# Optimization experiments

Hardware: AMD Instinct MI355X
Metric: run time of the kernel (lower is better)

## Reference

```python
import jax, jax.numpy as jnp
import numpy as np

DIM = 96
HEADS = 6
WS = 8                      # window_size
OWS = int(WS * 0.5) + WS    # overlap_win_size = 12
PAD = (OWS - WS) // 2       # 2
Dd = Hh = Ww = 24
B = 1
L = Dd * Hh * Ww
MLP_H = DIM * 2
TBL = (WS + OWS - 1) ** 3   # 6859 relative-position-bias entries


def setup_inputs() -> dict:
    key = jax.random.key(0)
    ks = jax.random.split(key, 8)
    def n(k, shape, s=0.02):
        return jax.random.normal(k, shape, jnp.float32) * s
    return {
        "x": jax.random.normal(ks[0], (B, L, DIM), jnp.float32),
        "ln1_w": jnp.ones((DIM,), jnp.float32),
        "ln1_b": jnp.zeros((DIM,), jnp.float32),
        "qkv_w": n(ks[1], (3 * DIM, DIM)),
        "qkv_b": jnp.zeros((3 * DIM,), jnp.float32),
        "rpb": n(ks[2], (TBL, HEADS)),
        "proj_w": n(ks[3], (DIM, DIM)),
        "proj_b": jnp.zeros((DIM,), jnp.float32),
        "ln2_w": jnp.ones((DIM,), jnp.float32),
        "ln2_b": jnp.zeros((DIM,), jnp.float32),
        "fc1_w": n(ks[4], (MLP_H, DIM)),
        "fc1_b": jnp.zeros((MLP_H,), jnp.float32),
        "fc2_w": n(ks[5], (DIM, MLP_H)),
        "fc2_b": jnp.zeros((DIM,), jnp.float32),
        "rpi": jax.random.randint(ks[6], (WS ** 3, OWS ** 3), 0, TBL),
        "D": Dd, "H": Hh, "W": Ww,
    }


def _ln(x, w, b):
    m = jnp.mean(x, -1, keepdims=True)
    v = jnp.var(x, -1, keepdims=True)
    return (x - m) / jnp.sqrt(v + 1e-5) * w + b


def _ocab3d(x, ln1_w, ln1_b, qkv_w, qkv_b, rpb, proj_w, proj_b,
            ln2_w, ln2_b, fc1_w, fc1_b, fc2_w, fc2_b, rpi, D, H, W):
    Bz, Lz, C = x.shape
    hd = C // HEADS
    scale = hd ** -0.5
    shortcut = x

    xn = _ln(x, ln1_w, ln1_b).reshape(Bz, D, H, W, C)
    qkv = xn @ qkv_w.T + qkv_b                   # [B,D,H,W,3C]
    q = qkv[..., :C]
    kv = qkv[..., C:]                            # cat(k, v) on channels, [B,D,H,W,2C]

    nD, nH, nW = D // WS, H // WS, W // WS
    nw = nD * nH * nW

    # non-overlapping query windows -> [B*nw, WS^3, C]
    qw = q.reshape(Bz, nD, WS, nH, WS, nW, WS, C)
    qw = qw.transpose(0, 1, 3, 5, 2, 4, 6, 7).reshape(Bz * nw, WS ** 3, C)

    # overlapping kv windows via pad + strided gather (mirrors F.pad + unfold)
    kvp = jnp.pad(kv, ((0, 0), (PAD, PAD), (PAD, PAD), (PAD, PAD), (0, 0)))
    idx_d = (jnp.arange(nD) * WS)[:, None] + jnp.arange(OWS)[None, :]
    idx_h = (jnp.arange(nH) * WS)[:, None] + jnp.arange(OWS)[None, :]
    idx_w = (jnp.arange(nW) * WS)[:, None] + jnp.arange(OWS)[None, :]
    kw = kvp[:, idx_d]                 # [B,nD,OWS,Hp,Wp,2C]
    kw = kw[:, :, :, idx_h]            # [B,nD,OWS,nH,OWS,Wp,2C]
    kw = kw[:, :, :, :, :, idx_w]      # [B,nD,OWS,nH,OWS,nW,OWS,2C]
    kw = kw.transpose(0, 1, 3, 5, 2, 4, 6, 7).reshape(Bz * nw, OWS ** 3, 2 * C)
    kk, vv = kw[..., :C], kw[..., C:]

    qh = qw.reshape(-1, WS ** 3, HEADS, hd).transpose(0, 2, 1, 3) * scale
    kh = kk.reshape(-1, OWS ** 3, HEADS, hd).transpose(0, 2, 1, 3)
    vh = vv.reshape(-1, OWS ** 3, HEADS, hd).transpose(0, 2, 1, 3)

    attn = jnp.einsum('bhqd,bhkd->bhqk', qh, kh)               # [B*nw,H,512,1728]
    bias = rpb[rpi.reshape(-1)].reshape(WS ** 3, OWS ** 3, HEADS).transpose(2, 0, 1)
    attn = jax.nn.softmax(attn + bias[None], axis=-1)
    out = jnp.einsum('bhqk,bhkd->bhqd', attn, vh)
    out = out.transpose(0, 2, 1, 3).reshape(Bz * nw, WS ** 3, C)

    # window reverse -> [B, L, C]
    out = out.reshape(Bz, nD, nH, nW, WS, WS, WS, C)
    out = out.transpose(0, 1, 4, 2, 5, 3, 6, 7).reshape(Bz, D * H * W, C)

    x2 = out @ proj_w.T + proj_b + shortcut
    h1 = jax.nn.gelu(_ln(x2, ln2_w, ln2_b) @ fc1_w.T + fc1_b, approximate=False)
    return x2 + (h1 @ fc2_w.T + fc2_b)


def reference(x, ln1_w, ln1_b, qkv_w, qkv_b, rpb, proj_w, proj_b,
              ln2_w, ln2_b, fc1_w, fc1_b, fc2_w, fc2_b, rpi, D, H, W):
    return _ocab3d(x, ln1_w, ln1_b, qkv_w, qkv_b, rpb, proj_w, proj_b,
                   ln2_w, ln2_b, fc1_w, fc1_b, fc2_w, fc2_b, rpi, D, H, W)
```

## Files before the change

### kernel.cpp

```cpp
#include <hip/hip_runtime.h>
#include <math.h>

#define DIMC   96
#define NHEADS 6
#define HD     16
#define WSZ    8
#define OWSZ   12
#define PADW   2
#define DD     24
#define LTOK   13824
#define NWIN   27
#define NKEY   1728
#define NROW   512
#define MLPH   192
#define PDIM   28
#define PD3    21952
#define KVPN   (NHEADS*PD3*32)
#define TBL    6859

typedef __attribute__((ext_vector_type(4))) short bf16x4;
typedef __attribute__((ext_vector_type(8))) short bf16x8;
typedef __attribute__((ext_vector_type(4))) float f32x4;

__device__ __forceinline__ unsigned short bfround(float f) {
    unsigned u = __float_as_uint(f);
    return (unsigned short)((u + 0x7FFFu + ((u >> 16) & 1u)) >> 16);
}
__device__ __forceinline__ unsigned bfpack(float a, float b) {
    unsigned ua = __float_as_uint(a), ub = __float_as_uint(b);
    ua = (ua + 0x7FFFu + ((ua >> 16) & 1u)) >> 16;
    ub = (ub + 0x7FFFu + ((ub >> 16) & 1u)) >> 16;
    return ua | (ub << 16);
}
__device__ __forceinline__ uint4 pack8(const float* v) {
    uint4 u;
    u.x = bfpack(v[0], v[1]); u.y = bfpack(v[2], v[3]);
    u.z = bfpack(v[4], v[5]); u.w = bfpack(v[6], v[7]);
    return u;
}
__device__ __forceinline__ bf16x4 pack4(f32x4 p) {
    union { uint2 u; bf16x4 v; } r;
    r.u.x = __builtin_amdgcn_perm(__float_as_uint(p[1]), __float_as_uint(p[0]), 0x07060302u);
    r.u.y = __builtin_amdgcn_perm(__float_as_uint(p[3]), __float_as_uint(p[2]), 0x07060302u);
    return r.v;
}
__device__ __forceinline__ f32x4 mfma16(bf16x4 a, bf16x4 b, f32x4 c) {
#if __has_builtin(__builtin_amdgcn_mfma_f32_16x16x16bf16_1k)
    return __builtin_amdgcn_mfma_f32_16x16x16bf16_1k(a, b, c, 0, 0, 0);
#else
    bf16x8 a8 = {a[0], a[1], a[2], a[3], 0, 0, 0, 0};
    bf16x8 b8 = {b[0], b[1], b[2], b[3], 0, 0, 0, 0};
    return __builtin_amdgcn_mfma_f32_16x16x32_bf16(a8, b8, c, 0, 0, 0);
#endif
}

__global__ void zero_kernel(float4* __restrict__ p, int n4) {
    int i = blockIdx.x * blockDim.x + threadIdx.x;
    if (i < n4) p[i] = make_float4(0.f, 0.f, 0.f, 0.f);
}

__global__ __launch_bounds__(256) void rpbT_kernel(
        const float* __restrict__ rpb, float* __restrict__ rpbT) {
    int i = blockIdx.x * 256 + threadIdx.x;
    if (i < TBL) {
        #pragma unroll
        for (int h = 0; h < NHEADS; ++h) rpbT[h * TBL + i] = rpb[i * NHEADS + h];
    }
}

template<int KT, int NCHUNKS, int MODE, bool LN>
__global__ __launch_bounds__(256) void gemm_kernel(
        const float* __restrict__ X, const float* __restrict__ W,
        const float* __restrict__ bias, const float* __restrict__ lnw,
        const float* __restrict__ lnb, const float* __restrict__ res,
        void* __restrict__ out, void* __restrict__ out2) {
    constexpr int K = KT * 32;
    __shared__ uint4 Af4[2 * KT * 4 * 16];
    __shared__ uint4 Bf4[6 * KT * 4 * 16];
    int tid  = threadIdx.x;
    int row0 = blockIdx.x * 32;

    if (tid < 128) {
        int row = tid >> 2, part = tid & 3;
        int rt = row >> 4, mm = row & 15;
        const float* xr = X + (long)(row0 + row) * K + part * (K / 4);
        if (LN) {
            float v[24];
            const float4* xp = (const float4*)xr;
            float s = 0.f, sq = 0.f;
            #pragma unroll
            for (int i = 0; i < 6; ++i) {
                float4 t = xp[i];
                v[i*4+0] = t.x; v[i*4+1] = t.y; v[i*4+2] = t.z; v[i*4+3] = t.w;
                s  += t.x + t.y + t.z + t.w;
                sq += t.x*t.x + t.y*t.y + t.z*t.z + t.w*t.w;
            }
            s  += __shfl_xor(s, 1);  s  += __shfl_xor(s, 2);
            sq += __shfl_xor(sq, 1); sq += __shfl_xor(sq, 2);
            float mean = s * (1.f / 96.f);
            float inv  = rsqrtf(sq * (1.f / 96.f) - mean * mean + 1e-5f);
            const float4* wp = (const float4*)(lnw + part * 24);
            const float4* bp = (const float4*)(lnb + part * 24);
            #pragma unroll
            for (int i = 0; i < 6; ++i) {
                float4 wv = wp[i], bv = bp[i];
                v[i*4+0] = (v[i*4+0] - mean) * inv * wv.x + bv.x;
                v[i*4+1] = (v[i*4+1] - mean) * inv * wv.y + bv.y;
                v[i*4+2] = (v[i*4+2] - mean) * inv * wv.z + bv.z;
                v[i*4+3] = (v[i*4+3] - mean) * inv * wv.w + bv.w;
            }
            #pragma unroll
            for (int gg = 0; gg < 3; ++gg) {
                int g = part * 3 + gg;
                int kt = g >> 2, qq = g & 3;
                Af4[((rt * KT + kt) * 4 + qq) * 16 + mm] = pack8(v + gg * 8);
            }
        } else {
            #pragma unroll
            for (int gg = 0; gg < KT; ++gg) {
                const float4* xp = (const float4*)(xr + gg * 8);
                float v[8];
                float4 t0 = xp[0], t1 = xp[1];
                v[0]=t0.x; v[1]=t0.y; v[2]=t0.z; v[3]=t0.w;
                v[4]=t1.x; v[5]=t1.y; v[6]=t1.z; v[7]=t1.w;
                int g = part * KT + gg;
                int kt = g >> 2, qq = g & 3;
                Af4[((rt * KT + kt) * 4 + qq) * 16 + mm] = pack8(v);
            }
        }
    }

    int wave = tid >> 6, lane = tid & 63;
    int qq = lane >> 4, mI = lane & 15;
    int rt = wave & 1, cg = wave >> 1;

    for (int nc = 0; nc < NCHUNKS; ++nc) {
        if (nc) __syncthreads();
        for (int idx = tid; idx < 96 * 4 * KT; idx += 256) {
            int n = idx / (4 * KT);
            int g = idx % (4 * KT);
            const float4* wp = (const float4*)(W + (long)(nc * 96 + n) * K + g * 8);
            float v[8];
            float4 t0 = wp[0], t1 = wp[1];
            v[0]=t0.x; v[1]=t0.y; v[2]=t0.z; v[3]=t0.w;
            v[4]=t1.x; v[5]=t1.y; v[6]=t1.z; v[7]=t1.w;
            int ct = n >> 4, nn = n & 15, kt = g >> 2, qg = g & 3;
            Bf4[((ct * KT + kt) * 4 + qg) * 16 + nn] = pack8(v);
        }
        __syncthreads();

        f32x4 acc[3];
        #pragma unroll
        for (int j = 0; j < 3; ++j) acc[j] = (f32x4){0.f, 0.f, 0.f, 0.f};
        #pragma unroll
        for (int kt = 0; kt < KT; ++kt) {
            bf16x8 a = *(const bf16x8*)&Af4[((rt * KT + kt) * 4 + qq) * 16 + mI];
            #pragma unroll
            for (int j = 0; j < 3; ++j) {
                bf16x8 b = *(const bf16x8*)&Bf4[(((cg * 3 + j) * KT + kt) * 4 + qq) * 16 + mI];
                acc[j] = __builtin_amdgcn_mfma_f32_16x16x32_bf16(a, b, acc[j], 0, 0, 0);
            }
        }

        float bv[3];
        #pragma unroll
        for (int j = 0; j < 3; ++j) bv[j] = bias[nc * 96 + (cg * 3 + j) * 16 + mI];
        #pragma unroll
        for (int r = 0; r < 4; ++r) {
            int row = row0 + rt * 16 + qq * 4 + r;
            if (MODE == 0) {
                if (nc == 0) {
                    unsigned short* op = (unsigned short*)out + (long)row * 96;
                    #pragma unroll
                    for (int j = 0; j < 3; ++j)
                        op[(cg * 3 + j) * 16 + mI] = bfround(0.25f * (acc[j][r] + bv[j]));
                } else {
                    int d = row / 576, hh = (row / 24) % 24, w2 = row % 24;
                    long pos = ((long)(d + 2) * 28 + (hh + 2)) * 28 + (w2 + 2);
                    #pragma unroll
                    for (int j = 0; j < 3; ++j) {
                        int head = cg * 3 + j;
                        ((unsigned short*)out2)[((long)head * PD3 + pos) * 32 +
                            (nc == 2 ? 16 : 0) + mI] = bfround(acc[j][r] + bv[j]);
                    }
                }
            } else if (MODE == 1 || MODE == 3) {
                const float* rp = res + (long)row * 96;
                float* op = (float*)out + (long)row * 96;
                #pragma unroll
                for (int j = 0; j < 3; ++j)
                    op[(cg * 3 + j) * 16 + mI] = acc[j][r] + bv[j] + rp[(cg * 3 + j) * 16 + mI];
            } else {
                float* op = (float*)out + (long)row * 192 + nc * 96;
                #pragma unroll
                for (int j = 0; j < 3; ++j) {
                    float v = acc[j][r] + bv[j];
                    op[(cg * 3 + j) * 16 + mI] = 0.5f * v * (1.f + erff(v * 0.70710678f));
                }
            }
        }
    }
}

__global__ __launch_bounds__(256) void bias_kernel(
        const int* __restrict__ rpi, const float* __restrict__ rpbT,
        unsigned short* __restrict__ biasP) {
    int b = blockIdx.x, head = b / 108, kt = b % 108;
    const float* tab = rpbT + head * TBL;
    int k0 = kt * 16;
    #pragma unroll
    for (int qq = 0; qq < 2; ++qq) {
        int qi = threadIdx.x * 2 + qq;
        const int* rp = rpi + (long)qi * NKEY + k0;
        int idx[16];
        #pragma unroll
        for (int j = 0; j < 4; ++j) {
            int4 t = *(const int4*)(rp + j * 4);
            idx[j*4+0] = t.x; idx[j*4+1] = t.y; idx[j*4+2] = t.z; idx[j*4+3] = t.w;
        }
        #pragma unroll
        for (int quad = 0; quad < 4; ++quad) {
            ushort4 v;
            v.x = bfround(tab[idx[quad*4+0]]);
            v.y = bfround(tab[idx[quad*4+1]]);
            v.z = bfround(tab[idx[quad*4+2]]);
            v.w = bfround(tab[idx[quad*4+3]]);
            *(ushort4*)(biasP + ((((long)head*108 + kt)*4 + quad)*512 + qi)*4) = v;
        }
    }
}

#define KSTR 20
#define VSTR 68
__global__ __launch_bounds__(256) void attn_kernel(
        const unsigned short* __restrict__ q, const unsigned short* __restrict__ kvp2,
        const unsigned short* __restrict__ biasP, float* __restrict__ ao) {
    __shared__ unsigned short Ks[2][64 * KSTR];
    __shared__ unsigned short Vs[2][16 * VSTR];
    int bid = blockIdx.x;
    int w = bid / 24, rem = bid % 24;
    int head = rem >> 2, quart = rem & 3;
    int wd8 = (w / 9) * 8, wh8 = ((w / 3) % 3) * 8, ww8 = (w % 3) * 8;
    int tid = threadIdx.x, wave = tid >> 6, lane = tid & 63;
    int quad = lane >> 4, m16 = lane & 15;
    int key = tid >> 2, part = tid & 3;

    auto kvaddr = [&](int c) -> const uint4* {
        int jg = c * 64 + key;
        int i = jg / 144, jh = (jg / 12) % 12, jw = jg % 12;
        long sp = ((long)(wd8 + i) * PDIM + (wh8 + jh)) * PDIM + (ww8 + jw);
        return (const uint4*)(kvp2 + ((long)head * PD3 + sp) * 32 + part * 8);
    };
    auto writeLDS = [&](int b, uint4 v) {
        if (part < 2) {
            *(uint2*)(&Ks[b][key * KSTR + part * 8])     = make_uint2(v.x, v.y);
            *(uint2*)(&Ks[b][key * KSTR + part * 8 + 4]) = make_uint2(v.z, v.w);
        } else {
            int d0 = (part - 2) * 8;
            Vs[b][(d0+0)*VSTR + key] = (unsigned short)(v.x);
            Vs[b][(d0+1)*VSTR + key] = (unsigned short)(v.x >> 16);
            Vs[b][(d0+2)*VSTR + key] = (unsigned short)(v.y);
            Vs[b][(d0+3)*VSTR + key] = (unsigned short)(v.y >> 16);
            Vs[b][(d0+4)*VSTR + key] = (unsigned short)(v.z);
            Vs[b][(d0+5)*VSTR + key] = (unsigned short)(v.z >> 16);
            Vs[b][(d0+6)*VSTR + key] = (unsigned short)(v.w);
            Vs[b][(d0+7)*VSTR + key] = (unsigned short)(v.w >> 16);
        }
    };

    int grow[2]; bf16x4 qf[2];
    #pragma unroll
    for (int qt = 0; qt < 2; ++qt) {
        int ql = quart * 128 + wave * 32 + qt * 16 + m16;
        int ld = ql >> 6, lh = (ql >> 3) & 7, lw = ql & 7;
        grow[qt] = ((wd8 + ld) * 24 + (wh8 + lh)) * 24 + (ww8 + lw);
        qf[qt] = *(const bf16x4*)(q + (long)grow[qt] * 96 + head * 16 + quad * 4);
    }

    const unsigned short* bbase = biasP + (long)head * 884736 + quad * 2048
                                 + ((quart * 128 + wave * 32 + m16) << 2);
    uint2 bcur[2][4];
    #pragma unroll
    for (int qt = 0; qt < 2; ++qt)
        #pragma unroll
        for (int kt = 0; kt < 4; ++kt)
            bcur[qt][kt] = *(const uint2*)(bbase + kt * 8192 + qt * 64);

    writeLDS(0, *kvaddr(0));

    f32x4 o[2];
    o[0] = (f32x4){0.f,0.f,0.f,0.f}; o[1] = (f32x4){0.f,0.f,0.f,0.f};
    float l[2] = {0.f, 0.f};
    uint4 stgn;

    #pragma unroll 1
    for (int c = 0; c < 27; ++c) {
        if (c + 1 < 27) stgn = *kvaddr(c + 1);
        __syncthreads();
        int b = c & 1;

        bf16x4 kf[4];
        #pragma unroll
        for (int kt = 0; kt < 4; ++kt)
            kf[kt] = *(const bf16x4*)(&Ks[b][(kt * 16 + m16) * KSTR + quad * 4]);

        f32x4 S[2][4];
        #pragma unroll
        for (int qt = 0; qt < 2; ++qt)
            #pragma unroll
            for (int kt = 0; kt < 4; ++kt) {
                uint2 bv = bcur[qt][kt];
                f32x4 ci;
                ci[0] = __uint_as_float(bv.x << 16);
                ci[1] = __uint_as_float(bv.x & 0xffff0000u);
                ci[2] = __uint_as_float(bv.y << 16);
                ci[3] = __uint_as_float(bv.y & 0xffff0000u);
                S[qt][kt] = mfma16(kf[kt], qf[qt], ci);
            }

        uint2 bnxt[2][4];
        if (c + 1 < 27) {
            const unsigned short* bp = bbase + (long)(c + 1) * 32768;
            #pragma unroll
            for (int qt = 0; qt < 2; ++qt)
                #pragma unroll
                for (int kt = 0; kt < 4; ++kt)
                    bnxt[qt][kt] = *(const uint2*)(bp + kt * 8192 + qt * 64);
        }

        #pragma unroll
        for (int qt = 0; qt < 2; ++qt) {
            float ls = 0.f;
            #pragma unroll
            for (int kt = 0; kt < 4; ++kt)
                #pragma unroll
                for (int r = 0; r < 4; ++r) {
                    float p = __expf(S[qt][kt][r]);
                    S[qt][kt][r] = p; ls += p;
                }
            l[qt] += ls;
        }

        #pragma unroll
        for (int kt = 0; kt < 4; ++kt) {
            bf16x4 vf = *(const bf16x4*)(&Vs[b][m16 * VSTR + kt * 16 + quad * 4]);
            o[0] = mfma16(vf, pack4(S[0][kt]), o[0]);
            o[1] = mfma16(vf, pack4(S[1][kt]), o[1]);
        }

        if (c + 1 < 27) writeLDS((c + 1) & 1, stgn);
        #pragma unroll
        for (int qt = 0; qt < 2; ++qt)
            #pragma unroll
            for (int kt = 0; kt < 4; ++kt) bcur[qt][kt] = bnxt[qt][kt];
    }

    #pragma unroll
    for (int qt = 0; qt < 2; ++qt) {
        float lq = l[qt];
        lq += __shfl_xor(lq, 16);
        lq += __shfl_xor(lq, 32);
        float inv = 1.f / lq;
        float4* op = (float4*)(ao + (long)grow[qt] * 96 + head * 16 + quad * 4);
        *op = make_float4(o[qt][0]*inv, o[qt][1]*inv, o[qt][2]*inv, o[qt][3]*inv);
    }
}

extern "C" void kernel_launch(void* const* d_in, const int* in_sizes, int n_in,
                              void* d_out, int out_size, void* d_ws, size_t ws_size,
                              hipStream_t stream) {
    const float* x     = (const float*)d_in[0];
    const float* ln1w  = (const float*)d_in[1];
    const float* ln1b  = (const float*)d_in[2];
    const float* qkvw  = (const float*)d_in[3];
    const float* qkvb  = (const float*)d_in[4];
    const float* rpb   = (const float*)d_in[5];
    const float* projw = (const float*)d_in[6];
    const float* projb = (const float*)d_in[7];
    const float* ln2w  = (const float*)d_in[8];
    const float* ln2b  = (const float*)d_in[9];
    const float* fc1w  = (const float*)d_in[10];
    const float* fc1b  = (const float*)d_in[11];
    const float* fc2w  = (const float*)d_in[12];
    const float* fc2b  = (const float*)d_in[13];
    const int*   rpi   = (const int*)d_in[14];
    float* outp = (float*)d_out;

    float* ws = (float*)d_ws;
    float*          ao    = ws;
    unsigned short* q16   = (unsigned short*)(ws + 1327104);
    unsigned short* kvp16 = (unsigned short*)(ws + 1990656);
    float*          hbuf  = ws + 4098048;
    unsigned short* biasP = (unsigned short*)hbuf;
    float*          rpbT  = ws + 6752256;
    float*          x2    = ao;

    {
        int n4 = KVPN * 2 / 16;
        zero_kernel<<<(n4 + 255) / 256, 256, 0, stream>>>((float4*)kvp16, n4);
    }
    rpbT_kernel<<<27, 256, 0, stream>>>(rpb, rpbT);
    gemm_kernel<3, 3, 0, true ><<<432, 256, 0, stream>>>(x,  qkvw, qkvb, ln1w, ln1b, nullptr, q16, kvp16);
    bias_kernel<<<NHEADS * 108, 256, 0, stream>>>(rpi, rpbT, biasP);
    attn_kernel<<<NWIN * NHEADS * 4, 256, 0, stream>>>(q16, kvp16, biasP, ao);
    gemm_kernel<3, 1, 1, false><<<432, 256, 0, stream>>>(ao, projw, projb, nullptr, nullptr, x, x2, nullptr);
    gemm_kernel<3, 2, 2, true ><<<432, 256, 0, stream>>>(x2, fc1w, fc1b, ln2w, ln2b, nullptr, hbuf, nullptr);
    gemm_kernel<6, 1, 3, false><<<432, 256, 0, stream>>>(hbuf, fc2w, fc2b, nullptr, nullptr, x2, outp, nullptr);
}
```

Measured before the change: 196.4 us.

## Split attention keys across two blocks and parallelize GEMM output chunks

The attention kernel now splits the 27 key chunks between two blocks per query tile. Each block writes an unnormalized output and row sums, and the projection GEMM combines the two halves and normalizes while loading its A tile. The gemm kernel moves its output-column chunks from a loop to separate blocks, the zero and rpb-transpose kernels merge into one launch, and the bias table is stored in fp32 instead of bf16. The aim is more blocks in flight and fewer launches, at the cost of doubled attention output traffic, a larger bias buffer, and repeated LN/A-tile loading per chunk.

Result: faster. 190.9 us (-2.8%).

```diff
diff --git a/kernel.cpp b/kernel.cpp
--- a/kernel.cpp
+++ b/kernel.cpp
@@ -17,6 +17,8 @@
 #define PD3    21952
 #define KVPN   (NHEADS*PD3*32)
 #define TBL    6859
+#define LSTR   82944
+#define AOSTR  1327104
 
 typedef __attribute__((ext_vector_type(4))) short bf16x4;
 typedef __attribute__((ext_vector_type(8))) short bf16x8;
@@ -54,39 +56,68 @@
 #endif
 }
 
-__global__ void zero_kernel(float4* __restrict__ p, int n4) {
-    int i = blockIdx.x * blockDim.x + threadIdx.x;
-    if (i < n4) p[i] = make_float4(0.f, 0.f, 0.f, 0.f);
-}
-
-__global__ __launch_bounds__(256) void rpbT_kernel(
-        const float* __restrict__ rpb, float* __restrict__ rpbT) {
-    int i = blockIdx.x * 256 + threadIdx.x;
-    if (i < TBL) {
-        #pragma unroll
-        for (int h = 0; h < NHEADS; ++h) rpbT[h * TBL + i] = rpb[i * NHEADS + h];
-    }
-}
-
-template<int KT, int NCHUNKS, int MODE, bool LN>
+#define ZBLK 2058
+__global__ __launch_bounds__(256) void init_kernel(
+        float4* __restrict__ kvz, const float* __restrict__ rpb,
+        float* __restrict__ rpbT) {
+    int bx = blockIdx.x;
+    if (bx < ZBLK) {
+        int i = bx * 256 + threadIdx.x;
+        if (i < KVPN * 2 / 16) kvz[i] = make_float4(0.f, 0.f, 0.f, 0.f);
+    } else {
+        int i = (bx - ZBLK) * 256 + threadIdx.x;
+        if (i < TBL) {
+            #pragma unroll
+            for (int h = 0; h < NHEADS; ++h) rpbT[h * TBL + i] = rpb[i * NHEADS + h];
+        }
+    }
+}
+
+template<int KT, int MODE, bool LN, int NSPLIT>
 __global__ __launch_bounds__(256) void gemm_kernel(
         const float* __restrict__ X, const float* __restrict__ W,
         const float* __restrict__ bias, const float* __restrict__ lnw,
         const float* __restrict__ lnb, const float* __restrict__ res,
+        const float* __restrict__ X2, const float* __restrict__ lbuf,
         void* __restrict__ out, void* __restrict__ out2) {
     constexpr int K = KT * 32;
     __shared__ uint4 Af4[2 * KT * 4 * 16];
     __shared__ uint4 Bf4[6 * KT * 4 * 16];
     int tid  = threadIdx.x;
-    int row0 = blockIdx.x * 32;
+    int nc   = blockIdx.x % NSPLIT;
+    int row0 = (blockIdx.x / NSPLIT) * 32;
 
     if (tid < 128) {
         int row = tid >> 2, part = tid & 3;
         int rt = row >> 4, mm = row & 15;
-        const float* xr = X + (long)(row0 + row) * K + part * (K / 4);
-        if (LN) {
+        if (MODE == 1) {
+            int grow = row0 + row;
+            const float4* a0 = (const float4*)(X  + (long)grow * 96 + part * 24);
+            const float4* a1 = (const float4*)(X2 + (long)grow * 96 + part * 24);
+            int ha = (part * 3) >> 1, hb = ha + 1;
+            float inva = 1.f / (lbuf[grow*6 + ha] + lbuf[LSTR + grow*6 + ha]);
+            float invb = 1.f / (lbuf[grow*6 + hb] + lbuf[LSTR + grow*6 + hb]);
             float v[24];
-            const float4* xp = (const float4*)xr;
+            #pragma unroll
+            for (int i = 0; i < 6; ++i) {
+                float4 u0 = a0[i], u1 = a1[i];
+                #pragma unroll
+                for (int j = 0; j < 4; ++j) {
+                    int gc = part * 24 + i * 4 + j;
+                    float lv = ((gc >> 4) == ha) ? inva : invb;
+                    float s = (j==0?u0.x+u1.x : j==1?u0.y+u1.y : j==2?u0.z+u1.z : u0.w+u1.w);
+                    v[i*4+j] = s * lv;
+                }
+            }
+            #pragma unroll
+            for (int gg = 0; gg < 3; ++gg) {
+                int g = part * 3 + gg;
+                int kt = g >> 2, qq = g & 3;
+                Af4[((rt * KT + kt) * 4 + qq) * 16 + mm] = pack8(v + gg * 8);
+            }
+        } else if (LN) {
+            float v[24];
+            const float4* xp = (const float4*)(X + (long)(row0 + row) * K + part * 24);
             float s = 0.f, sq = 0.f;
             #pragma unroll
             for (int i = 0; i < 6; ++i) {
@@ -116,6 +147,7 @@
                 Af4[((rt * KT + kt) * 4 + qq) * 16 + mm] = pack8(v + gg * 8);
             }
         } else {
+            const float* xr = X + (long)(row0 + row) * K + part * (K / 4);
             #pragma unroll
             for (int gg = 0; gg < KT; ++gg) {
                 const float4* xp = (const float4*)(xr + gg * 8);
@@ -130,73 +162,70 @@
         }
     }
 
+    for (int idx = tid; idx < 96 * 4 * KT; idx += 256) {
+        int n = idx / (4 * KT);
+        int g = idx % (4 * KT);
+        const float4* wp = (const float4*)(W + (long)(nc * 96 + n) * K + g * 8);
+        float v[8];
+        float4 t0 = wp[0], t1 = wp[1];
+        v[0]=t0.x; v[1]=t0.y; v[2]=t0.z; v[3]=t0.w;
+        v[4]=t1.x; v[5]=t1.y; v[6]=t1.z; v[7]=t1.w;
+        int ct = n >> 4, nn = n & 15, kt = g >> 2, qg = g & 3;
+        Bf4[((ct * KT + kt) * 4 + qg) * 16 + nn] = pack8(v);
+    }
+    __syncthreads();
+
     int wave = tid >> 6, lane = tid & 63;
     int qq = lane >> 4, mI = lane & 15;
     int rt = wave & 1, cg = wave >> 1;
 
-    for (int nc = 0; nc < NCHUNKS; ++nc) {
-        if (nc) __syncthreads();
-        for (int idx = tid; idx < 96 * 4 * KT; idx += 256) {
-            int n = idx / (4 * KT);
-            int g = idx % (4 * KT);
-            const float4* wp = (const float4*)(W + (long)(nc * 96 + n) * K + g * 8);
-            float v[8];
-            float4 t0 = wp[0], t1 = wp[1];
-            v[0]=t0.x; v[1]=t0.y; v[2]=t0.z; v[3]=t0.w;
-            v[4]=t1.x; v[5]=t1.y; v[6]=t1.z; v[7]=t1.w;
-            int ct = n >> 4, nn = n & 15, kt = g >> 2, qg = g & 3;
-            Bf4[((ct * KT + kt) * 4 + qg) * 16 + nn] = pack8(v);
-        }
-        __syncthreads();
-
-        f32x4 acc[3];
-        #pragma unroll
-        for (int j = 0; j < 3; ++j) acc[j] = (f32x4){0.f, 0.f, 0.f, 0.f};
-        #pragma unroll
-        for (int kt = 0; kt < KT; ++kt) {
-            bf16x8 a = *(const bf16x8*)&Af4[((rt * KT + kt) * 4 + qq) * 16 + mI];
-            #pragma unroll
-            for (int j = 0; j < 3; ++j) {
-                bf16x8 b = *(const bf16x8*)&Bf4[(((cg * 3 + j) * KT + kt) * 4 + qq) * 16 + mI];
-                acc[j] = __builtin_amdgcn_mfma_f32_16x16x32_bf16(a, b, acc[j], 0, 0, 0);
-            }
-        }
-
-        float bv[3];
-        #pragma unroll
-        for (int j = 0; j < 3; ++j) bv[j] = bias[nc * 96 + (cg * 3 + j) * 16 + mI];
-        #pragma unroll
-        for (int r = 0; r < 4; ++r) {
-            int row = row0 + rt * 16 + qq * 4 + r;
-            if (MODE == 0) {
-                if (nc == 0) {
-                    unsigned short* op = (unsigned short*)out + (long)row * 96;
-                    #pragma unroll
-                    for (int j = 0; j < 3; ++j)
-                        op[(cg * 3 + j) * 16 + mI] = bfround(0.25f * (acc[j][r] + bv[j]));
-                } else {
-                    int d = row / 576, hh = (row / 24) % 24, w2 = row % 24;
-                    long pos = ((long)(d + 2) * 28 + (hh + 2)) * 28 + (w2 + 2);
-                    #pragma unroll
-                    for (int j = 0; j < 3; ++j) {
-                        int head = cg * 3 + j;
-                        ((unsigned short*)out2)[((long)head * PD3 + pos) * 32 +
-                            (nc == 2 ? 16 : 0) + mI] = bfround(acc[j][r] + bv[j]);
-                    }
-                }
-            } else if (MODE == 1 || MODE == 3) {
-                const float* rp = res + (long)row * 96;
-                float* op = (float*)out + (long)row * 96;
+    f32x4 acc[3];
+    #pragma unroll
+    for (int j = 0; j < 3; ++j) acc[j] = (f32x4){0.f, 0.f, 0.f, 0.f};
+    #pragma unroll
+    for (int kt = 0; kt < KT; ++kt) {
+        bf16x8 a = *(const bf16x8*)&Af4[((rt * KT + kt) * 4 + qq) * 16 + mI];
+        #pragma unroll
+        for (int j = 0; j < 3; ++j) {
+            bf16x8 b = *(const bf16x8*)&Bf4[(((cg * 3 + j) * KT + kt) * 4 + qq) * 16 + mI];
+            acc[j] = __builtin_amdgcn_mfma_f32_16x16x32_bf16(a, b, acc[j], 0, 0, 0);
+        }
+    }
+
+    float bv[3];
+    #pragma unroll
+    for (int j = 0; j < 3; ++j) bv[j] = bias[nc * 96 + (cg * 3 + j) * 16 + mI];
+    #pragma unroll
+    for (int r = 0; r < 4; ++r) {
+        int row = row0 + rt * 16 + qq * 4 + r;
+        if (MODE == 0) {
+            if (nc == 0) {
+                unsigned short* op = (unsigned short*)out + (long)row * 96;
                 #pragma unroll
                 for (int j = 0; j < 3; ++j)
-                    op[(cg * 3 + j) * 16 + mI] = acc[j][r] + bv[j] + rp[(cg * 3 + j) * 16 + mI];
+                    op[(cg * 3 + j) * 16 + mI] = bfround(0.25f * (acc[j][r] + bv[j]));
             } else {
-                float* op = (float*)out + (long)row * 192 + nc * 96;
+                int d = row / 576, hh = (row / 24) % 24, w2 = row % 24;
+                long pos = ((long)(d + 2) * 28 + (hh + 2)) * 28 + (w2 + 2);
                 #pragma unroll
                 for (int j = 0; j < 3; ++j) {
-                    float v = acc[j][r] + bv[j];
-                    op[(cg * 3 + j) * 16 + mI] = 0.5f * v * (1.f + erff(v * 0.70710678f));
+                    int head = cg * 3 + j;
+                    ((unsigned short*)out2)[((long)head * PD3 + pos) * 32 +
+                        (nc == 2 ? 16 : 0) + mI] = bfround(acc[j][r] + bv[j]);
                 }
+            }
+        } else if (MODE == 1 || MODE == 3) {
+            const float* rp = res + (long)row * 96;
+            float* op = (float*)out + (long)row * 96;
+            #pragma unroll
+            for (int j = 0; j < 3; ++j)
+                op[(cg * 3 + j) * 16 + mI] = acc[j][r] + bv[j] + rp[(cg * 3 + j) * 16 + mI];
+        } else {
+            float* op = (float*)out + (long)row * 192 + nc * 96;
+            #pragma unroll
+            for (int j = 0; j < 3; ++j) {
+                float v = acc[j][r] + bv[j];
+                op[(cg * 3 + j) * 16 + mI] = 0.5f * v * (1.f + erff(v * 0.70710678f));
             }
         }
     }
@@ -204,29 +233,29 @@
 
 __global__ __launch_bounds__(256) void bias_kernel(
         const int* __restrict__ rpi, const float* __restrict__ rpbT,
-        unsigned short* __restrict__ biasP) {
-    int b = blockIdx.x, head = b / 108, kt = b % 108;
+        float* __restrict__ biasP) {
+    int bx = blockIdx.x;
+    int head = bx / 216;
+    int r2 = bx % 216;
+    int kt = r2 >> 1, qh = r2 & 1;
     const float* tab = rpbT + head * TBL;
     int k0 = kt * 16;
-    #pragma unroll
-    for (int qq = 0; qq < 2; ++qq) {
-        int qi = threadIdx.x * 2 + qq;
-        const int* rp = rpi + (long)qi * NKEY + k0;
-        int idx[16];
-        #pragma unroll
-        for (int j = 0; j < 4; ++j) {
-            int4 t = *(const int4*)(rp + j * 4);
-            idx[j*4+0] = t.x; idx[j*4+1] = t.y; idx[j*4+2] = t.z; idx[j*4+3] = t.w;
-        }
-        #pragma unroll
-        for (int quad = 0; quad < 4; ++quad) {
-            ushort4 v;
-            v.x = bfround(tab[idx[quad*4+0]]);
-            v.y = bfround(tab[idx[quad*4+1]]);
-            v.z = bfround(tab[idx[quad*4+2]]);
-            v.w = bfround(tab[idx[quad*4+3]]);
-            *(ushort4*)(biasP + ((((long)head*108 + kt)*4 + quad)*512 + qi)*4) = v;
-        }
+    int qi = qh * 256 + threadIdx.x;
+    const int* rp = rpi + (long)qi * NKEY + k0;
+    int idx[16];
+    #pragma unroll
+    for (int j = 0; j < 4; ++j) {
+        int4 t = *(const int4*)(rp + j * 4);
+        idx[j*4+0] = t.x; idx[j*4+1] = t.y; idx[j*4+2] = t.z; idx[j*4+3] = t.w;
+    }
+    #pragma unroll
+    for (int quad = 0; quad < 4; ++quad) {
+        float4 v;
+        v.x = tab[idx[quad*4+0]];
+        v.y = tab[idx[quad*4+1]];
+        v.z = tab[idx[quad*4+2]];
+        v.w = tab[idx[quad*4+3]];
+        *(float4*)(biasP + ((((long)head*108 + kt)*4 + quad)*512 + qi)*4) = v;
     }
 }
 
@@ -234,16 +263,20 @@
 #define VSTR 68
 __global__ __launch_bounds__(256) void attn_kernel(
         const unsigned short* __restrict__ q, const unsigned short* __restrict__ kvp2,
-        const unsigned short* __restrict__ biasP, float* __restrict__ ao) {
+        const float* __restrict__ biasP, float* __restrict__ ao,
+        float* __restrict__ lbuf) {
     __shared__ unsigned short Ks[2][64 * KSTR];
     __shared__ unsigned short Vs[2][16 * VSTR];
     int bid = blockIdx.x;
-    int w = bid / 24, rem = bid % 24;
-    int head = rem >> 2, quart = rem & 3;
+    int w = bid / 48, rem = bid % 48;
+    int head = rem >> 3;
+    int quart = (rem >> 1) & 3, half = rem & 1;
     int wd8 = (w / 9) * 8, wh8 = ((w / 3) % 3) * 8, ww8 = (w % 3) * 8;
     int tid = threadIdx.x, wave = tid >> 6, lane = tid & 63;
     int quad = lane >> 4, m16 = lane & 15;
     int key = tid >> 2, part = tid & 3;
+    int c0 = half ? 13 : 0;
+    int cn = half ? 14 : 13;
 
     auto kvaddr = [&](int c) -> const uint4* {
         int jg = c * 64 + key;
@@ -277,16 +310,16 @@
         qf[qt] = *(const bf16x4*)(q + (long)grow[qt] * 96 + head * 16 + quad * 4);
     }
 
-    const unsigned short* bbase = biasP + (long)head * 884736 + quad * 2048
-                                 + ((quart * 128 + wave * 32 + m16) << 2);
-    uint2 bcur[2][4];
+    const float* bbase = biasP + (long)head * 884736 + quad * 2048
+                         + ((quart * 128 + wave * 32 + m16) << 2);
+    f32x4 bcur[2][4];
     #pragma unroll
     for (int qt = 0; qt < 2; ++qt)
         #pragma unroll
         for (int kt = 0; kt < 4; ++kt)
-            bcur[qt][kt] = *(const uint2*)(bbase + kt * 8192 + qt * 64);
-
-    writeLDS(0, *kvaddr(0));
+            bcur[qt][kt] = *(const f32x4*)(bbase + (long)(c0*4 + kt) * 8192 + qt * 64);
+
+    writeLDS(0, *kvaddr(c0));
 
     f32x4 o[2];
     o[0] = (f32x4){0.f,0.f,0.f,0.f}; o[1] = (f32x4){0.f,0.f,0.f,0.f};
@@ -294,10 +327,11 @@
     uint4 stgn;
 
     #pragma unroll 1
-    for (int c = 0; c < 27; ++c) {
-        if (c + 1 < 27) stgn = *kvaddr(c + 1);
+    for (int cc = 0; cc < cn; ++cc) {
+        int c = c0 + cc;
+        if (cc + 1 < cn) stgn = *kvaddr(c + 1);
         __syncthreads();
-        int b = c & 1;
+        int b = cc & 1;
 
         bf16x4 kf[4];
         #pragma unroll
@@ -308,24 +342,17 @@
         #pragma unroll
         for (int qt = 0; qt < 2; ++qt)
             #pragma unroll
-            for (int kt = 0; kt < 4; ++kt) {
-                uint2 bv = bcur[qt][kt];
-                f32x4 ci;
-                ci[0] = __uint_as_float(bv.x << 16);
-                ci[1] = __uint_as_float(bv.x & 0xffff0000u);
-                ci[2] = __uint_as_float(bv.y << 16);
-                ci[3] = __uint_as_float(bv.y & 0xffff0000u);
-                S[qt][kt] = mfma16(kf[kt], qf[qt], ci);
-            }
-
-        uint2 bnxt[2][4];
-        if (c + 1 < 27) {
-            const unsigned short* bp = bbase + (long)(c + 1) * 32768;
+            for (int kt = 0; kt < 4; ++kt)
+                S[qt][kt] = mfma16(kf[kt], qf[qt], bcur[qt][kt]);
+
+        f32x4 bnxt[2][4];
+        if (cc + 1 < cn) {
+            const float* bp = bbase + (long)(c + 1) * 32768;
             #pragma unroll
             for (int qt = 0; qt < 2; ++qt)
                 #pragma unroll
                 for (int kt = 0; kt < 4; ++kt)
-                    bnxt[qt][kt] = *(const uint2*)(bp + kt * 8192 + qt * 64);
+                    bnxt[qt][kt] = *(const f32x4*)(bp + kt * 8192 + qt * 64);
         }
 
         #pragma unroll
@@ -348,21 +375,23 @@
             o[1] = mfma16(vf, pack4(S[1][kt]), o[1]);
         }
 
-        if (c + 1 < 27) writeLDS((c + 1) & 1, stgn);
+        if (cc + 1 < cn) writeLDS((cc + 1) & 1, stgn);
         #pragma unroll
         for (int qt = 0; qt < 2; ++qt)
             #pragma unroll
             for (int kt = 0; kt < 4; ++kt) bcur[qt][kt] = bnxt[qt][kt];
     }
 
+    float* aout = ao + (long)half * AOSTR;
+    float* lout = lbuf + (long)half * LSTR;
     #pragma unroll
     for (int qt = 0; qt < 2; ++qt) {
         float lq = l[qt];
         lq += __shfl_xor(lq, 16);
         lq += __shfl_xor(lq, 32);
-        float inv = 1.f / lq;
-        float4* op = (float4*)(ao + (long)grow[qt] * 96 + head * 16 + quad * 4);
-        *op = make_float4(o[qt][0]*inv, o[qt][1]*inv, o[qt][2]*inv, o[qt][3]*inv);
+        float4* op = (float4*)(aout + (long)grow[qt] * 96 + head * 16 + quad * 4);
+        *op = make_float4(o[qt][0], o[qt][1], o[qt][2], o[qt][3]);
+        if (quad == 0) lout[grow[qt] * 6 + head] = lq;
     }
 }
 
@@ -387,23 +416,20 @@
     float* outp = (float*)d_out;
 
     float* ws = (float*)d_ws;
-    float*          ao    = ws;
-    unsigned short* q16   = (unsigned short*)(ws + 1327104);
-    unsigned short* kvp16 = (unsigned short*)(ws + 1990656);
-    float*          hbuf  = ws + 4098048;
-    unsigned short* biasP = (unsigned short*)hbuf;
-    float*          rpbT  = ws + 6752256;
-    float*          x2    = ao;
-
-    {
-        int n4 = KVPN * 2 / 16;
-        zero_kernel<<<(n4 + 255) / 256, 256, 0, stream>>>((float4*)kvp16, n4);
-    }
-    rpbT_kernel<<<27, 256, 0, stream>>>(rpb, rpbT);
-    gemm_kernel<3, 3, 0, true ><<<432, 256, 0, stream>>>(x,  qkvw, qkvb, ln1w, ln1b, nullptr, q16, kvp16);
-    bias_kernel<<<NHEADS * 108, 256, 0, stream>>>(rpi, rpbT, biasP);
-    attn_kernel<<<NWIN * NHEADS * 4, 256, 0, stream>>>(q16, kvp16, biasP, ao);
-    gemm_kernel<3, 1, 1, false><<<432, 256, 0, stream>>>(ao, projw, projb, nullptr, nullptr, x, x2, nullptr);
-    gemm_kernel<3, 2, 2, true ><<<432, 256, 0, stream>>>(x2, fc1w, fc1b, ln2w, ln2b, nullptr, hbuf, nullptr);
-    gemm_kernel<6, 1, 3, false><<<432, 256, 0, stream>>>(hbuf, fc2w, fc2b, nullptr, nullptr, x2, outp, nullptr);
-}
+    float*          aop    = ws;
+    unsigned short* q16    = (unsigned short*)(ws + 2654208);
+    unsigned short* kvp16  = (unsigned short*)(ws + 3317760);
+    float*          biasPf = ws + 5425152;
+    float*          hbuf   = biasPf;
+    float*          rpbT   = ws + 10733568;
+    float*          lbuf   = ws + 10774722;
+    float*          x2     = aop;
+
+    init_kernel<<<ZBLK + 27, 256, 0, stream>>>((float4*)kvp16, rpb, rpbT);
+    gemm_kernel<3, 0, true , 3><<<1296, 256, 0, stream>>>(x,  qkvw, qkvb, ln1w, ln1b, nullptr, nullptr, nullptr, q16, kvp16);
+    bias_kernel<<<1296, 256, 0, stream>>>(rpi, rpbT, biasPf);
+    attn_kernel<<<NWIN * NHEADS * 4 * 2, 256, 0, stream>>>(q16, kvp16, biasPf, aop, lbuf);
+    gemm_kernel<3, 1, false, 1><<<432, 256, 0, stream>>>(aop, projw, projb, nullptr, nullptr, x, aop + AOSTR, lbuf, x2, nullptr);
+    gemm_kernel<3, 2, true , 2><<<864, 256, 0, stream>>>(x2, fc1w, fc1b, ln2w, ln2b, nullptr, nullptr, nullptr, hbuf, nullptr);
+    gemm_kernel<6, 3, false, 1><<<432, 256, 0, stream>>>(hbuf, fc2w, fc2b, nullptr, nullptr, x2, nullptr, nullptr, outp, nullptr);
+}
```
